# Kernel optimization log

Measured on AMD Instinct MI355X. Metric: run time of the kernel, lower is better.

## Reference

```python
import jax, jax.numpy as jnp
import numpy as np

DIM = 240; NH = 6; HD = 20          # dim, num_heads, head_dim = dim // (2*num_heads)
WS = 16; BWS = 8                    # window size, base window size
R = (WS // BWS) ** 2                # spatial_linear in_features (=4)
LW = WS * WS; LB = BWS * BWS

# static relative-position index for a WSxWS window (same construction as torch buffer)
_coords = np.stack(np.meshgrid(np.arange(WS), np.arange(WS), indexing='ij')).reshape(2, -1)
_rel = (_coords[:, :, None] - _coords[:, None, :]).transpose(1, 2, 0).astype(np.int64)
_rel[..., 0] += WS - 1; _rel[..., 1] += WS - 1; _rel[..., 0] *= 2 * WS - 1
RPI = jnp.asarray(_rel.sum(-1))     # [LW, LW]


def conv2d(x, w, b, pad):
    y = jax.lax.conv_general_dilated(x, w, (1, 1), [(pad, pad), (pad, pad)],
                                     dimension_numbers=('NCHW', 'OIHW', 'NCHW'))
    return y + b[None, :, None, None]


def lrelu(x):
    return jnp.where(x >= 0, x, 0.2 * x)  # LeakyReLU(0.2)


def layer_norm(x, g, b, eps=1e-5):
    m = x.mean(-1, keepdims=True)
    v = jnp.mean((x - m) ** 2, axis=-1, keepdims=True)
    return (x - m) * jax.lax.rsqrt(v + eps) * g + b


def setup_inputs() -> dict:
    key = jax.random.key(0)
    ks = iter(jax.random.split(key, 40))
    rn = lambda shape: jax.random.normal(next(ks), shape, jnp.float32) * 0.02
    B, H, W = 2, 256, 256
    pd = (DIM // 4) // 4  # DynamicPosBias pos_dim = 15
    return {
        'x': jax.random.normal(next(ks), (B, H * W, DIM), jnp.float32),
        # DFE (qv projection)
        'c1_w': rn((DIM // 5, DIM, 1, 1)), 'c1_b': jnp.zeros((DIM // 5,), jnp.float32),
        'c2_w': rn((DIM // 5, DIM // 5, 3, 3)), 'c2_b': jnp.zeros((DIM // 5,), jnp.float32),
        'c3_w': rn((DIM, DIM // 5, 1, 1)), 'c3_b': jnp.zeros((DIM,), jnp.float32),
        'lin_w': rn((DIM, DIM, 1, 1)), 'lin_b': jnp.zeros((DIM,), jnp.float32),
        # spatial linear projection Linear(R, 1)
        'sl_w': rn((1, R)), 'sl_b': jnp.zeros((1,), jnp.float32),
        # DynamicPosBias MLP (residual=False)
        'pp_w': rn((pd, 2)), 'pp_b': jnp.zeros((pd,), jnp.float32),
        'ln1_g': jnp.ones((pd,), jnp.float32), 'ln1_b': jnp.zeros((pd,), jnp.float32),
        'p1_w': rn((pd, pd)), 'p1_b': jnp.zeros((pd,), jnp.float32),
        'ln2_g': jnp.ones((pd,), jnp.float32), 'ln2_b': jnp.zeros((pd,), jnp.float32),
        'p2_w': rn((pd, pd)), 'p2_b': jnp.zeros((pd,), jnp.float32),
        'ln3_g': jnp.ones((pd,), jnp.float32), 'ln3_b': jnp.zeros((pd,), jnp.float32),
        'p3_w': rn((NH, pd)), 'p3_b': jnp.zeros((NH,), jnp.float32),
        # output projection
        'proj_w': rn((DIM, DIM)), 'proj_b': jnp.zeros((DIM,), jnp.float32),
        'H': 256, 'W': 256,
    }


def reference(x, c1_w, c1_b, c2_w, c2_b, c3_w, c3_b, lin_w, lin_b, sl_w, sl_b,
              pp_w, pp_b, ln1_g, ln1_b, p1_w, p1_b, ln2_g, ln2_b, p2_w, p2_b,
              ln3_g, ln3_b, p3_w, p3_b, proj_w, proj_b, H, W):
    B, L, C = x.shape
    # ---- DFE feature projection (conv-gated) ----
    xi = jnp.transpose(x, (0, 2, 1)).reshape(B, C, H, W)
    conv = conv2d(lrelu(conv2d(lrelu(conv2d(xi, c1_w, c1_b, 0)), c2_w, c2_b, 1)), c3_w, c3_b, 0)
    qv = conv * conv2d(xi, lin_w, lin_b, 0)                       # [B,C,H,W]
    qv = jnp.transpose(qv, (0, 2, 3, 1))                          # [B,H,W,C]
    # ---- window partition ----
    nh_w, nw_w = H // WS, W // WS
    qv = qv.reshape(B, nh_w, WS, nw_w, WS, C).transpose(0, 1, 3, 2, 4, 5).reshape(-1, LW, C)
    B_ = qv.shape[0]
    qv = qv.reshape(B_, LW, 2, NH, HD).transpose(2, 0, 3, 1, 4)   # [2,B_,NH,LW,HD]
    q, v = qv[0], qv[1]
    # ---- spatial self-correlation ----
    # spatial linear projection of v: [B_,NH,LW,HD] -> [B_,NH,LB,HD]
    vs = v.reshape(B_, NH, BWS, WS // BWS, BWS, WS // BWS, HD)
    vs = vs.transpose(0, 1, 2, 4, 6, 3, 5).reshape(B_, NH, LB, HD, R)
    vs = jnp.einsum('bnkcr,or->bnkc', vs, sl_w) + sl_b            # Linear(R,1), squeezed
    corr = jnp.einsum('bnlc,bnkc->bnlk', q, vs) / HD              # [B_,NH,LW,LB]
    # dynamic relative position bias (MLP over the mother set of relative coords)
    ph = jnp.arange(1 - WS, WS)
    biases = jnp.stack(jnp.meshgrid(ph, ph, indexing='ij')).reshape(2, -1).T.astype(x.dtype)
    pos = biases @ pp_w.T + pp_b
    pos = jax.nn.relu(layer_norm(pos, ln1_g, ln1_b)) @ p1_w.T + p1_b
    pos = jax.nn.relu(layer_norm(pos, ln2_g, ln2_b)) @ p2_w.T + p2_b
    pos = jax.nn.relu(layer_norm(pos, ln3_g, ln3_b)) @ p3_w.T + p3_b  # [(2*WS-1)^2, NH]
    rpb = jnp.take(pos, RPI.reshape(-1), axis=0).reshape(LW, LW, NH).transpose(2, 0, 1)
    # pool key axis to base-window resolution (consistent with spatial_linear_projection grouping)
    rpb = rpb.reshape(NH, LW, BWS, WS // BWS, BWS, WS // BWS).mean((3, 5)).reshape(NH, LW, LB)
    corr = corr + rpb[None]
    x_s = jnp.einsum('bnlk,bnkc->bnlc', corr, vs)
    x_s = x_s.transpose(0, 2, 1, 3).reshape(B_, LW, NH * HD)      # [B_,LW,C/2]
    # ---- channel self-correlation (single-head over merged channels) ----
    qc = q.transpose(0, 2, 1, 3).reshape(B_, LW, NH * HD)
    vc = v.transpose(0, 2, 1, 3).reshape(B_, LW, NH * HD)
    corr_c = jnp.einsum('blc,bld->bcd', qc, vc) / LW              # [B_,C/2,C/2]
    x_c = jnp.einsum('bcd,bld->blc', corr_c, vc)                  # [B_,LW,C/2]
    # ---- window reverse + spatial-channel fusion ----
    def wrev(t):
        return t.reshape(B, nh_w, nw_w, WS, WS, -1).transpose(0, 1, 3, 2, 4, 5).reshape(B, H, W, -1)
    out = jnp.concatenate([wrev(x_s), wrev(x_c)], axis=-1)        # [B,H,W,C]
    out = out @ proj_w.T + proj_b
    return out.reshape(B, L, C)
```

## Files before the change

kernel.cpp:

```cpp
#include <hip/hip_runtime.h>
#include <math.h>

#define NPIX 131072

typedef __attribute__((ext_vector_type(8))) short bfrag;
typedef __attribute__((ext_vector_type(4))) float facc;
typedef __attribute__((ext_vector_type(4))) unsigned short us4;

__device__ __forceinline__ float lrelu_f(float x) { return x >= 0.f ? x : 0.2f * x; }

__device__ __forceinline__ int pix_of(int w, int l) {
    int b = w >> 8, wi = (w >> 4) & 15, wj = w & 15;
    return ((((b << 4) + wi) * 16 + (l >> 4)) << 8) + (wj << 4) + (l & 15);
}

__device__ __forceinline__ unsigned short bf16rn(float f) {
    unsigned u = __builtin_bit_cast(unsigned, f);
    u += 0x7FFFu + ((u >> 16) & 1u);
    return (unsigned short)(u >> 16);
}
__device__ __forceinline__ float bf16tof(unsigned short h) {
    unsigned u = ((unsigned)h) << 16;
    return __builtin_bit_cast(float, u);
}

__global__ __launch_bounds__(256) void split_x_kernel(const float* __restrict__ x,
                                                      unsigned short* __restrict__ xs2)
{
    int idx = blockIdx.x * 256 + threadIdx.x;
    int row = idx >> 5;
    int k = (idx & 31) * 8;
    float v[8];
    if (k < 240) {
        float4 a = *(const float4*)(x + (size_t)row * 240 + k);
        float4 b = *(const float4*)(x + (size_t)row * 240 + k + 4);
        v[0] = a.x; v[1] = a.y; v[2] = a.z; v[3] = a.w;
        v[4] = b.x; v[5] = b.y; v[6] = b.z; v[7] = b.w;
    } else {
#pragma unroll
        for (int e = 0; e < 8; ++e) v[e] = 0.f;
    }
    bfrag hi, lo;
#pragma unroll
    for (int e = 0; e < 8; ++e) {
        unsigned short h = bf16rn(v[e]);
        hi[e] = (short)h;
        lo[e] = (short)bf16rn(v[e] - bf16tof(h));
    }
    unsigned short* dst = xs2 + (size_t)row * 512 + k;
    *(bfrag*)(dst) = hi;
    *(bfrag*)(dst + 256) = lo;
}

__global__ __launch_bounds__(256) void pack_w_kernel(const float* __restrict__ src,
                                                     int rows, int K,
                                                     unsigned short* __restrict__ dst,
                                                     int total8, int KPAD)
{
    int idx = blockIdx.x * 256 + threadIdx.x;
    if (idx >= total8) return;
    int kper = KPAD >> 3;
    int row = idx / kper;
    int k = (idx - row * kper) * 8;
    float v[8];
#pragma unroll
    for (int e = 0; e < 8; ++e) {
        int kk = k + e;
        v[e] = (row < rows && kk < K) ? src[(size_t)row * K + kk] : 0.f;
    }
    bfrag hi, lo;
#pragma unroll
    for (int e = 0; e < 8; ++e) {
        unsigned short h = bf16rn(v[e]);
        hi[e] = (short)h;
        lo[e] = (short)bf16rn(v[e] - bf16tof(h));
    }
    unsigned short* d = dst + (size_t)row * 2 * KPAD + k;
    *(bfrag*)(d) = hi;
    *(bfrag*)(d + KPAD) = lo;
}

__global__ __launch_bounds__(256) void pack_c2w_kernel(const float* __restrict__ c2_w,
                                                       unsigned short* __restrict__ c2w2)
{
    int idx = blockIdx.x * 256 + threadIdx.x;
    if (idx >= 6912) return;
    int rowid = idx >> 4;
    int c = idx & 15;
    int tap = rowid / 48, n = rowid - tap * 48;
    int ty = tap / 3, tx = tap - ty * 3;
    int lohalf = c >> 3;
    int cbase = (c & 7) * 8;
    bfrag outv;
#pragma unroll
    for (int e = 0; e < 8; ++e) {
        int ci = cbase + e;
        float v = (ci < 48) ? c2_w[(((size_t)n * 48 + ci) * 3 + ty) * 3 + tx] : 0.f;
        unsigned short h = bf16rn(v);
        outv[e] = (short)(lohalf ? bf16rn(v - bf16tof(h)) : h);
    }
    *(bfrag*)(c2w2 + (size_t)rowid * 128 + c * 8) = outv;
}

__device__ __forceinline__ void ln_relu15(const float* h, float* r,
                                          const float* __restrict__ g,
                                          const float* __restrict__ b) {
    float m = 0.f;
#pragma unroll
    for (int f = 0; f < 15; ++f) m += h[f];
    m *= (1.f / 15.f);
    float v = 0.f;
#pragma unroll
    for (int f = 0; f < 15; ++f) { float d = h[f] - m; v += d * d; }
    float rs = rsqrtf(v * (1.f / 15.f) + 1e-5f);
#pragma unroll
    for (int f = 0; f < 15; ++f) {
        float xx = (h[f] - m) * rs * g[f] + b[f];
        r[f] = xx > 0.f ? xx : 0.f;
    }
}

__device__ __forceinline__ void lin15(const float* r, float* h,
                                      const float* __restrict__ w,
                                      const float* __restrict__ b) {
#pragma unroll
    for (int o = 0; o < 15; ++o) {
        float s = b[o];
#pragma unroll
        for (int g = 0; g < 15; ++g) s += r[g] * w[o * 15 + g];
        h[o] = s;
    }
}

__global__ __launch_bounds__(256) void prep_pos_kernel(
    const float* __restrict__ pp_w, const float* __restrict__ pp_b,
    const float* __restrict__ ln1_g, const float* __restrict__ ln1_b,
    const float* __restrict__ p1_w, const float* __restrict__ p1_b,
    const float* __restrict__ ln2_g, const float* __restrict__ ln2_b,
    const float* __restrict__ p2_w, const float* __restrict__ p2_b,
    const float* __restrict__ ln3_g, const float* __restrict__ ln3_b,
    const float* __restrict__ p3_w, const float* __restrict__ p3_b,
    float* __restrict__ pos3)
{
    int tid = threadIdx.x;
    for (int idx = tid; idx < 961; idx += 256) {
        float h[15], r[15];
        float in0 = (float)(idx / 31) - 15.f;
        float in1 = (float)(idx % 31) - 15.f;
#pragma unroll
        for (int f = 0; f < 15; ++f) h[f] = in0 * pp_w[2 * f] + in1 * pp_w[2 * f + 1] + pp_b[f];
        ln_relu15(h, r, ln1_g, ln1_b);
        lin15(r, h, p1_w, p1_b);
        ln_relu15(h, r, ln2_g, ln2_b);
        lin15(r, h, p2_w, p2_b);
        ln_relu15(h, r, ln3_g, ln3_b);
#pragma unroll
        for (int o = 0; o < 6; ++o) {
            float s = p3_b[o];
#pragma unroll
            for (int g = 0; g < 15; ++g) s += r[g] * p3_w[o * 15 + g];
            pos3[idx * 6 + o] = s;
        }
    }
}

__global__ __launch_bounds__(256) void rpb_kernel(const float* __restrict__ pos3,
                                                  float* __restrict__ rpb_t)
{
    int out = blockIdx.x * 256 + threadIdx.x;
    int n = out >> 14;
    int k = (out >> 8) & 63;
    int l = out & 255;
    int a = k >> 3, c = k & 7;
    int i1 = l >> 4, j1 = l & 15;
    float s = 0.f;
#pragma unroll
    for (int bb = 0; bb < 2; ++bb)
#pragma unroll
        for (int d = 0; d < 2; ++d) {
            int i2 = a * 2 + bb, j2 = c * 2 + d;
            int rpi = (i1 - i2 + 15) * 31 + (j1 - j2 + 15);
            s += pos3[rpi * 6 + n];
        }
    rpb_t[out] = s * 0.25f;
}

__device__ __forceinline__ void mfma_kpass3(const unsigned short* __restrict__ A2, int lda2,
                                            const unsigned short* __restrict__ W2, int ldw2,
                                            int ksteps, int mbase, int nbase,
                                            short* lds_a, short* lds_w,
                                            int tid, int wm, int wn,
                                            facc acc[4][4])
{
    int lane = tid & 63;
    int i = lane & 15, g = lane >> 4;
    int kpa = lda2 >> 1, kpw = ldw2 >> 1;
    for (int s = 0; s < ksteps; ++s) {
        int k0 = s * 32;
        {
            int r = tid >> 1, h16 = (tid & 1) * 16;
            const unsigned short* src = A2 + (size_t)(mbase + r) * lda2 + k0 + h16;
            bfrag h0 = *(const bfrag*)(src);
            bfrag h1 = *(const bfrag*)(src + 8);
            bfrag l0 = *(const bfrag*)(src + kpa);
            bfrag l1 = *(const bfrag*)(src + kpa + 8);
            short* dst = lds_a + r * 72 + h16;
            *(bfrag*)(dst)      = h0;  *(bfrag*)(dst + 8)  = h1;
            *(bfrag*)(dst + 32) = l0;  *(bfrag*)(dst + 40) = l1;
        }
        {
            int r = tid >> 1, half = tid & 1;
            const unsigned short* src = W2 + (size_t)(nbase + r) * ldw2 + half * kpw + k0;
            bfrag v0 = *(const bfrag*)(src);
            bfrag v1 = *(const bfrag*)(src + 8);
            bfrag v2 = *(const bfrag*)(src + 16);
            bfrag v3 = *(const bfrag*)(src + 24);
            short* dst = lds_w + r * 72 + half * 32;
            *(bfrag*)(dst)      = v0;  *(bfrag*)(dst + 8)  = v1;
            *(bfrag*)(dst + 16) = v2;  *(bfrag*)(dst + 24) = v3;
        }
        __syncthreads();
        bfrag ah[4], al[4], bh[4], bl[4];
#pragma unroll
        for (int mu = 0; mu < 4; ++mu) {
            const short* p = lds_a + (wm * 64 + mu * 16 + i) * 72 + g * 8;
            ah[mu] = *(const bfrag*)(p);
            al[mu] = *(const bfrag*)(p + 32);
        }
#pragma unroll
        for (int nu = 0; nu < 4; ++nu) {
            const short* p = lds_w + (wn * 64 + nu * 16 + i) * 72 + g * 8;
            bh[nu] = *(const bfrag*)(p);
            bl[nu] = *(const bfrag*)(p + 32);
        }
#pragma unroll
        for (int mu = 0; mu < 4; ++mu)
#pragma unroll
            for (int nu = 0; nu < 4; ++nu) {
                acc[mu][nu] = __builtin_amdgcn_mfma_f32_16x16x32_bf16(ah[mu], bh[nu], acc[mu][nu], 0, 0, 0);
                acc[mu][nu] = __builtin_amdgcn_mfma_f32_16x16x32_bf16(ah[mu], bl[nu], acc[mu][nu], 0, 0, 0);
                acc[mu][nu] = __builtin_amdgcn_mfma_f32_16x16x32_bf16(al[mu], bh[nu], acc[mu][nu], 0, 0, 0);
            }
        __syncthreads();
    }
}

__device__ __forceinline__ void mfma_kpass_n64(const unsigned short* __restrict__ A2, int lda2,
                                               const unsigned short* __restrict__ W2, int ldw2,
                                               int ksteps, int mbase,
                                               short* lds_a, short* lds_w,
                                               int tid, int wm, int wn,
                                               facc acc[4][2])
{
    int lane = tid & 63;
    int i = lane & 15, g = lane >> 4;
    int kpa = lda2 >> 1, kpw = ldw2 >> 1;
    for (int s = 0; s < ksteps; ++s) {
        int k0 = s * 32;
        {
            int r = tid >> 1, h16 = (tid & 1) * 16;
            const unsigned short* src = A2 + (size_t)(mbase + r) * lda2 + k0 + h16;
            bfrag h0 = *(const bfrag*)(src);
            bfrag h1 = *(const bfrag*)(src + 8);
            bfrag l0 = *(const bfrag*)(src + kpa);
            bfrag l1 = *(const bfrag*)(src + kpa + 8);
            short* dst = lds_a + r * 72 + h16;
            *(bfrag*)(dst)      = h0;  *(bfrag*)(dst + 8)  = h1;
            *(bfrag*)(dst + 32) = l0;  *(bfrag*)(dst + 40) = l1;
        }
        if (tid < 128) {
            int r = tid >> 1, half = tid & 1;
            const unsigned short* src = W2 + (size_t)r * ldw2 + half * kpw + k0;
            bfrag v0 = *(const bfrag*)(src);
            bfrag v1 = *(const bfrag*)(src + 8);
            bfrag v2 = *(const bfrag*)(src + 16);
            bfrag v3 = *(const bfrag*)(src + 24);
            short* dst = lds_w + r * 72 + half * 32;
            *(bfrag*)(dst)      = v0;  *(bfrag*)(dst + 8)  = v1;
            *(bfrag*)(dst + 16) = v2;  *(bfrag*)(dst + 24) = v3;
        }
        __syncthreads();
        bfrag ah[4], al[4], bh[2], bl[2];
#pragma unroll
        for (int mu = 0; mu < 4; ++mu) {
            const short* p = lds_a + (wm * 64 + mu * 16 + i) * 72 + g * 8;
            ah[mu] = *(const bfrag*)(p);
            al[mu] = *(const bfrag*)(p + 32);
        }
#pragma unroll
        for (int nu = 0; nu < 2; ++nu) {
            const short* p = lds_w + (wn * 32 + nu * 16 + i) * 72 + g * 8;
            bh[nu] = *(const bfrag*)(p);
            bl[nu] = *(const bfrag*)(p + 32);
        }
#pragma unroll
        for (int mu = 0; mu < 4; ++mu)
#pragma unroll
            for (int nu = 0; nu < 2; ++nu) {
                acc[mu][nu] = __builtin_amdgcn_mfma_f32_16x16x32_bf16(ah[mu], bh[nu], acc[mu][nu], 0, 0, 0);
                acc[mu][nu] = __builtin_amdgcn_mfma_f32_16x16x32_bf16(ah[mu], bl[nu], acc[mu][nu], 0, 0, 0);
                acc[mu][nu] = __builtin_amdgcn_mfma_f32_16x16x32_bf16(al[mu], bh[nu], acc[mu][nu], 0, 0, 0);
            }
        __syncthreads();
    }
}

__global__ __launch_bounds__(256) void conv1_mfma_kernel(const unsigned short* __restrict__ xs2,
    const unsigned short* __restrict__ c1_w2, const float* __restrict__ bias,
    unsigned short* __restrict__ t1s)
{
    __shared__ __align__(16) short lds_a[128 * 72];
    __shared__ __align__(16) short lds_w[64 * 72];
    int tid = threadIdx.x;
    int lane = tid & 63, wid = tid >> 6;
    int wm = wid >> 1, wn = wid & 1;
    int mbase = blockIdx.x * 128;
    facc zero = {0.f, 0.f, 0.f, 0.f};
    facc acc[4][2];
#pragma unroll
    for (int mu = 0; mu < 4; ++mu)
#pragma unroll
        for (int nu = 0; nu < 2; ++nu) acc[mu][nu] = zero;

    mfma_kpass_n64(xs2, 512, c1_w2, 512, 8, mbase, lds_a, lds_w, tid, wm, wn, acc);

    int i = lane & 15, g = lane >> 4;
#pragma unroll
    for (int nu = 0; nu < 2; ++nu) {
        int n = wn * 32 + nu * 16 + i;
        if (n < 48) {
            float bv = bias[n];
#pragma unroll
            for (int mu = 0; mu < 4; ++mu)
#pragma unroll
                for (int rr = 0; rr < 4; ++rr) {
                    size_t m = (size_t)mbase + wm * 64 + mu * 16 + g * 4 + rr;
                    float v = lrelu_f(acc[mu][nu][rr] + bv);
                    unsigned short h = bf16rn(v);
                    t1s[m * 128 + n] = h;
                    t1s[m * 128 + 64 + n] = bf16rn(v - bf16tof(h));
                }
        }
    }
    if (tid < 128) {
        size_t m = (size_t)mbase + tid;
        bfrag z = {0, 0, 0, 0, 0, 0, 0, 0};
        *(bfrag*)(t1s + m * 128 + 48)  = z;
        *(bfrag*)(t1s + m * 128 + 56)  = z;
        *(bfrag*)(t1s + m * 128 + 112) = z;
        *(bfrag*)(t1s + m * 128 + 120) = z;
    }
}

__global__ __launch_bounds__(256) void conv2_mfma_kernel(const unsigned short* __restrict__ t1s,
    const unsigned short* __restrict__ c2w2, const float* __restrict__ bias,
    unsigned short* __restrict__ t2s)
{
    __shared__ __align__(16) short a_s[130 * 128];
    int bid = blockIdx.x;
    int b = bid >> 9;
    int r = (bid >> 1) & 255;
    int half = bid & 1;
    int c0 = half * 128;
    int tid = threadIdx.x;
    int lane = tid & 63, wid = tid >> 6;
    int i = lane & 15, g = lane >> 4;
    facc zero = {0.f, 0.f, 0.f, 0.f};
    facc acc[2][3];
#pragma unroll
    for (int mu = 0; mu < 2; ++mu)
#pragma unroll
        for (int nu = 0; nu < 3; ++nu) acc[mu][nu] = zero;

    for (int dy = 0; dy < 3; ++dy) {
        int grow = r + dy - 1;
        bool rowok = (grow >= 0 && grow < 256);
        for (int idx = tid; idx < 130 * 16; idx += 256) {
            int j = idx >> 4, ch = idx & 15;
            int gc = c0 - 1 + j;
            bfrag v = {0, 0, 0, 0, 0, 0, 0, 0};
            if (rowok && gc >= 0 && gc < 256) {
                size_t gpix = ((size_t)b * 256 + grow) * 256 + gc;
                v = *(const bfrag*)(t1s + gpix * 128 + ch * 8);
            }
            *(bfrag*)&a_s[j * 128 + ((ch ^ (j & 7)) * 8)] = v;
        }
        __syncthreads();
#pragma unroll
        for (int dx = 0; dx < 3; ++dx) {
            const unsigned short* wb = c2w2 + (size_t)(dy * 3 + dx) * 48 * 128;
#pragma unroll
            for (int h = 0; h < 2; ++h) {
                bfrag ah[2], al[2], bh[3], bl[3];
#pragma unroll
                for (int mu = 0; mu < 2; ++mu) {
                    int j = wid * 32 + mu * 16 + i + dx;
                    int chi = (h * 4 + g) ^ (j & 7);
                    int clo = (8 + h * 4 + g) ^ (j & 7);
                    ah[mu] = *(const bfrag*)&a_s[j * 128 + chi * 8];
                    al[mu] = *(const bfrag*)&a_s[j * 128 + clo * 8];
                }
#pragma unroll
                for (int nu = 0; nu < 3; ++nu) {
                    const unsigned short* wp = wb + (size_t)(nu * 16 + i) * 128 + h * 32 + g * 8;
                    bh[nu] = *(const bfrag*)(wp);
                    bl[nu] = *(const bfrag*)(wp + 64);
                }
#pragma unroll
                for (int mu = 0; mu < 2; ++mu)
#pragma unroll
                    for (int nu = 0; nu < 3; ++nu) {
                        acc[mu][nu] = __builtin_amdgcn_mfma_f32_16x16x32_bf16(ah[mu], bh[nu], acc[mu][nu], 0, 0, 0);
                        acc[mu][nu] = __builtin_amdgcn_mfma_f32_16x16x32_bf16(ah[mu], bl[nu], acc[mu][nu], 0, 0, 0);
                        acc[mu][nu] = __builtin_amdgcn_mfma_f32_16x16x32_bf16(al[mu], bh[nu], acc[mu][nu], 0, 0, 0);
                    }
            }
        }
        __syncthreads();
    }
#pragma unroll
    for (int nu = 0; nu < 3; ++nu) {
        int n = nu * 16 + i;
        float bv = bias[n];
#pragma unroll
        for (int mu = 0; mu < 2; ++mu)
#pragma unroll
            for (int rr = 0; rr < 4; ++rr) {
                int lp = wid * 32 + mu * 16 + g * 4 + rr;
                size_t gpix = ((size_t)b * 256 + r) * 256 + (c0 + lp);
                float v = lrelu_f(acc[mu][nu][rr] + bv);
                unsigned short h = bf16rn(v);
                t2s[gpix * 128 + n] = h;
                t2s[gpix * 128 + 64 + n] = bf16rn(v - bf16tof(h));
            }
    }
    if (tid < 128) {
        size_t gpix = ((size_t)b * 256 + r) * 256 + (c0 + tid);
        bfrag z = {0, 0, 0, 0, 0, 0, 0, 0};
        *(bfrag*)(t2s + gpix * 128 + 48)  = z;
        *(bfrag*)(t2s + gpix * 128 + 56)  = z;
        *(bfrag*)(t2s + gpix * 128 + 112) = z;
        *(bfrag*)(t2s + gpix * 128 + 120) = z;
    }
}

__global__ __launch_bounds__(256) void qv_mfma_kernel(const unsigned short* __restrict__ xs2,
    const unsigned short* __restrict__ lin_w2, const float* __restrict__ lin_b,
    const unsigned short* __restrict__ t2s, const unsigned short* __restrict__ c3_w2,
    const float* __restrict__ c3_b, float* __restrict__ qv)
{
    __shared__ __align__(16) short lds_a[128 * 72];
    __shared__ __align__(16) short lds_w[128 * 72];
    int tid = threadIdx.x;
    int lane = tid & 63, wid = tid >> 6;
    int wm = wid >> 1, wn = wid & 1;
    int bid = blockIdx.y * 2 + blockIdx.x;
    int xcd = bid & 7, j = bid >> 3;
    int mbase = (xcd * 128 + (j >> 1)) * 128;
    int nbase = (j & 1) * 128;
    facc zero = {0.f, 0.f, 0.f, 0.f};
    facc acc1[4][4], acc2[4][4];
#pragma unroll
    for (int mu = 0; mu < 4; ++mu)
#pragma unroll
        for (int nu = 0; nu < 4; ++nu) { acc1[mu][nu] = zero; acc2[mu][nu] = zero; }

    mfma_kpass3(xs2, 512, lin_w2, 512, 8, mbase, nbase, lds_a, lds_w, tid, wm, wn, acc1);
    mfma_kpass3(t2s, 128, c3_w2, 128, 2, mbase, nbase, lds_a, lds_w, tid, wm, wn, acc2);

    int i = lane & 15, g = lane >> 4;
#pragma unroll
    for (int nu = 0; nu < 4; ++nu) {
        int n = nbase + wn * 64 + nu * 16 + i;
        if (n < 240) {
            float lb = lin_b[n], cb = c3_b[n];
#pragma unroll
            for (int mu = 0; mu < 4; ++mu)
#pragma unroll
                for (int rr = 0; rr < 4; ++rr) {
                    size_t m = (size_t)mbase + wm * 64 + mu * 16 + g * 4 + rr;
                    qv[m * 240 + n] = (acc2[mu][nu][rr] + cb) * (acc1[mu][nu][rr] + lb);
                }
        }
    }
}

__global__ __launch_bounds__(256) void proj_mfma_kernel(const unsigned short* __restrict__ cat2,
    const unsigned short* __restrict__ proj_w2, const float* __restrict__ bias,
    float* __restrict__ out)
{
    __shared__ __align__(16) short lds_a[128 * 72];
    __shared__ __align__(16) short lds_w[128 * 72];
    int tid = threadIdx.x;
    int lane = tid & 63, wid = tid >> 6;
    int wm = wid >> 1, wn = wid & 1;
    int bid = blockIdx.y * 2 + blockIdx.x;
    int xcd = bid & 7, j = bid >> 3;
    int mbase = (xcd * 128 + (j >> 1)) * 128;
    int nbase = (j & 1) * 128;
    facc zero = {0.f, 0.f, 0.f, 0.f};
    facc acc[4][4];
#pragma unroll
    for (int mu = 0; mu < 4; ++mu)
#pragma unroll
        for (int nu = 0; nu < 4; ++nu) acc[mu][nu] = zero;

    mfma_kpass3(cat2, 512, proj_w2, 512, 8, mbase, nbase, lds_a, lds_w, tid, wm, wn, acc);

    int i = lane & 15, g = lane >> 4;
#pragma unroll
    for (int nu = 0; nu < 4; ++nu) {
        int n = nbase + wn * 64 + nu * 16 + i;
        if (n < 240) {
            float bv = bias[n];
#pragma unroll
            for (int mu = 0; mu < 4; ++mu)
#pragma unroll
                for (int rr = 0; rr < 4; ++rr) {
                    size_t m = (size_t)mbase + wm * 64 + mu * 16 + g * 4 + rr;
                    out[m * 240 + n] = acc[mu][nu][rr] + bv;
                }
        }
    }
}

__global__ __launch_bounds__(256) void xs_kernel(const float* __restrict__ qv,
    const float* __restrict__ rpb_t, const float* __restrict__ sl_w,
    const float* __restrict__ sl_b, unsigned short* __restrict__ cat2)
{
    __shared__ __align__(16) float v_s[256 * 20];
    __shared__ __align__(16) float vs_s[64 * 20];
    int bid = blockIdx.x;
    int xcd = bid & 7;
    int j = bid >> 3;
    int wl = j / 6;
    int n = j - wl * 6;
    int w = xcd * 64 + wl;
    int tid = threadIdx.x;
    int l = tid;
    size_t pix = (size_t)pix_of(w, l);
    const float* qp = qv + pix * 240 + n * 20;
    float qr[20];
#pragma unroll
    for (int h4 = 0; h4 < 5; ++h4) {
        *(float4*)&qr[h4 * 4] = *(const float4*)(qp + h4 * 4);
        *(float4*)&v_s[l * 20 + h4 * 4] = *(const float4*)(qp + 120 + h4 * 4);
    }
    __syncthreads();
    float slw0 = sl_w[0], slw1 = sl_w[1], slw2 = sl_w[2], slw3 = sl_w[3];
    float slb = sl_b[0];
    for (int idx = tid; idx < 1280; idx += 256) {
        int k = idx / 20, hd = idx % 20;
        int a = k >> 3, c = k & 7;
        int l00 = a * 32 + c * 2;
        float vsum = slb
                   + slw0 * v_s[(l00 + 0) * 20 + hd]
                   + slw1 * v_s[(l00 + 1) * 20 + hd]
                   + slw2 * v_s[(l00 + 16) * 20 + hd]
                   + slw3 * v_s[(l00 + 17) * 20 + hd];
        vs_s[idx] = vsum;
    }
    __syncthreads();
    const float* rp = rpb_t + (size_t)n * 16384 + l;
    float acc[20];
#pragma unroll
    for (int hd = 0; hd < 20; ++hd) acc[hd] = 0.f;
#pragma unroll
    for (int k = 0; k < 64; ++k) {
        float vr[20];
#pragma unroll
        for (int h4 = 0; h4 < 5; ++h4)
            *(float4*)&vr[h4 * 4] = *(const float4*)&vs_s[k * 20 + h4 * 4];
        float s0 = 0.f, s1 = 0.f, s2 = 0.f, s3 = 0.f;
#pragma unroll
        for (int hd = 0; hd < 20; hd += 4) {
            s0 += qr[hd + 0] * vr[hd + 0];
            s1 += qr[hd + 1] * vr[hd + 1];
            s2 += qr[hd + 2] * vr[hd + 2];
            s3 += qr[hd + 3] * vr[hd + 3];
        }
        float cc = (s0 + s1 + s2 + s3) * (1.f / 20.f) + rp[(size_t)k * 256];
#pragma unroll
        for (int hd = 0; hd < 20; ++hd) acc[hd] += cc * vr[hd];
    }
    unsigned short* op = cat2 + pix * 512 + n * 20;
#pragma unroll
    for (int h4 = 0; h4 < 5; ++h4) {
        us4 h, lo;
#pragma unroll
        for (int e = 0; e < 4; ++e) {
            float v = acc[h4 * 4 + e];
            unsigned short hh = bf16rn(v);
            h[e] = hh;
            lo[e] = bf16rn(v - bf16tof(hh));
        }
        *(us4*)(op + h4 * 4) = h;
        *(us4*)(op + 256 + h4 * 4) = lo;
    }
    if (n == 0) {
        bfrag z = {0, 0, 0, 0, 0, 0, 0, 0};
        unsigned short* zp = cat2 + pix * 512;
        *(bfrag*)(zp + 240) = z;  *(bfrag*)(zp + 248) = z;
        *(bfrag*)(zp + 496) = z;  *(bfrag*)(zp + 504) = z;
    }
}

__global__ __launch_bounds__(256) void corrc_kernel(const float* __restrict__ qv,
                                                    float* __restrict__ G)
{
    __shared__ __align__(16) float vc_s[16 * 124];
    __shared__ __align__(16) float qc_s[16 * 124];
    int bid = blockIdx.x;
    int w = (bid & 7) * 64 + (bid >> 3);
    int tid = threadIdx.x, ty = tid >> 4, tx = tid & 15;
    float acc[8][8] = {};
    for (int l0 = 0; l0 < 256; l0 += 16) {
        for (int idx = tid; idx < 480; idx += 256) {
            int k = idx / 30, c4 = idx % 30;
            size_t pix = (size_t)pix_of(w, l0 + k);
            const float* qp = qv + pix * 240;
            *(float4*)&qc_s[k * 124 + c4 * 4] = *(const float4*)(qp + c4 * 4);
            *(float4*)&vc_s[k * 124 + c4 * 4] = *(const float4*)(qp + 120 + c4 * 4);
        }
        __syncthreads();
#pragma unroll
        for (int k = 0; k < 16; ++k) {
            float4 a0 = *(const float4*)&vc_s[k * 124 + ty * 8];
            float4 a1 = *(const float4*)&vc_s[k * 124 + ty * 8 + 4];
            float4 b0 = *(const float4*)&qc_s[k * 124 + tx * 8];
            float4 b1 = *(const float4*)&qc_s[k * 124 + tx * 8 + 4];
            float av[8] = {a0.x, a0.y, a0.z, a0.w, a1.x, a1.y, a1.z, a1.w};
            float bv[8] = {b0.x, b0.y, b0.z, b0.w, b1.x, b1.y, b1.z, b1.w};
#pragma unroll
            for (int i = 0; i < 8; ++i)
#pragma unroll
                for (int j = 0; j < 8; ++j) acc[i][j] += av[i] * bv[j];
        }
        __syncthreads();
    }
    float* gp = G + (size_t)w * 14400;
#pragma unroll
    for (int i = 0; i < 8; ++i) {
        int d = ty * 8 + i;
        if (d < 120) {
#pragma unroll
            for (int j4 = 0; j4 < 2; ++j4) {
                int c = tx * 8 + j4 * 4;
                if (c < 120) {
                    float4 o;
                    o.x = acc[i][j4 * 4 + 0]; o.y = acc[i][j4 * 4 + 1];
                    o.z = acc[i][j4 * 4 + 2]; o.w = acc[i][j4 * 4 + 3];
                    *(float4*)(gp + (size_t)d * 120 + c) = o;
                }
            }
        }
    }
}

__global__ __launch_bounds__(256) void xc_kernel(const float* __restrict__ qv,
    const float* __restrict__ G, unsigned short* __restrict__ cat2)
{
    __shared__ __align__(16) float a_s[8 * 132];
    __shared__ __align__(16) float b_s[8 * 124];
    int bid = blockIdx.x;
    int xcd = bid & 7, j = bid >> 3;
    int w = xcd * 64 + (j >> 1);
    int mh = j & 1;
    int tid = threadIdx.x, ty = tid >> 4, tx = tid & 15;
    const float* gp = G + (size_t)w * 14400;
    float acc[8][8] = {};
    for (int k0 = 0; k0 < 120; k0 += 8) {
        {
            int lloc = tid >> 1;
            int kk = (tid & 1) * 4;
            int l = mh * 128 + lloc;
            size_t pix = (size_t)pix_of(w, l);
            float4 v = *(const float4*)(qv + pix * 240 + 120 + k0 + kk);
            a_s[(kk + 0) * 132 + lloc] = v.x;
            a_s[(kk + 1) * 132 + lloc] = v.y;
            a_s[(kk + 2) * 132 + lloc] = v.z;
            a_s[(kk + 3) * 132 + lloc] = v.w;
        }
        if (tid < 240) {
            int k = tid / 30, c4 = tid % 30;
            *(float4*)&b_s[k * 124 + c4 * 4] =
                *(const float4*)(gp + (size_t)(k0 + k) * 120 + c4 * 4);
        }
        __syncthreads();
#pragma unroll
        for (int k = 0; k < 8; ++k) {
            float4 a0 = *(const float4*)&a_s[k * 132 + ty * 8];
            float4 a1 = *(const float4*)&a_s[k * 132 + ty * 8 + 4];
            float4 b0 = *(const float4*)&b_s[k * 124 + tx * 8];
            float4 b1 = *(const float4*)&b_s[k * 124 + tx * 8 + 4];
            float av[8] = {a0.x, a0.y, a0.z, a0.w, a1.x, a1.y, a1.z, a1.w};
            float bv[8] = {b0.x, b0.y, b0.z, b0.w, b1.x, b1.y, b1.z, b1.w};
#pragma unroll
            for (int i = 0; i < 8; ++i)
#pragma unroll
                for (int j2 = 0; j2 < 8; ++j2) acc[i][j2] += av[i] * bv[j2];
        }
        __syncthreads();
    }
#pragma unroll
    for (int i = 0; i < 8; ++i) {
        int l = mh * 128 + ty * 8 + i;
        size_t pix = (size_t)pix_of(w, l);
        unsigned short* op = cat2 + pix * 512;
#pragma unroll
        for (int j4 = 0; j4 < 2; ++j4) {
            int c = tx * 8 + j4 * 4;
            if (c < 120) {
                us4 h, lo;
#pragma unroll
                for (int e = 0; e < 4; ++e) {
                    float v = acc[i][j4 * 4 + e] * (1.f / 256.f);
                    unsigned short hh = bf16rn(v);
                    h[e] = hh;
                    lo[e] = bf16rn(v - bf16tof(hh));
                }
                *(us4*)(op + 120 + c) = h;
                *(us4*)(op + 256 + 120 + c) = lo;
            }
        }
    }
}

extern "C" void kernel_launch(void* const* d_in, const int* in_sizes, int n_in,
                              void* d_out, int out_size, void* d_ws, size_t ws_size,
                              hipStream_t stream)
{
    (void)in_sizes; (void)n_in; (void)out_size;
    const float* x     = (const float*)d_in[0];
    const float* c1_w  = (const float*)d_in[1];
    const float* c1_b  = (const float*)d_in[2];
    const float* c2_w  = (const float*)d_in[3];
    const float* c2_b  = (const float*)d_in[4];
    const float* c3_w  = (const float*)d_in[5];
    const float* c3_b  = (const float*)d_in[6];
    const float* lin_w = (const float*)d_in[7];
    const float* lin_b = (const float*)d_in[8];
    const float* sl_w  = (const float*)d_in[9];
    const float* sl_b  = (const float*)d_in[10];
    const float* pp_w  = (const float*)d_in[11];
    const float* pp_b  = (const float*)d_in[12];
    const float* ln1_g = (const float*)d_in[13];
    const float* ln1_b = (const float*)d_in[14];
    const float* p1_w  = (const float*)d_in[15];
    const float* p1_b  = (const float*)d_in[16];
    const float* ln2_g = (const float*)d_in[17];
    const float* ln2_b = (const float*)d_in[18];
    const float* p2_w  = (const float*)d_in[19];
    const float* p2_b  = (const float*)d_in[20];
    const float* ln3_g = (const float*)d_in[21];
    const float* ln3_b = (const float*)d_in[22];
    const float* p3_w  = (const float*)d_in[23];
    const float* p3_b  = (const float*)d_in[24];
    const float* proj_w = (const float*)d_in[25];
    const float* proj_b = (const float*)d_in[26];

    float* ws = (float*)d_ws;
    float* pos3   = ws;
    float* rpb_t  = ws + 8192;
    unsigned short* lin_w2  = (unsigned short*)(ws + 106496);
    unsigned short* c3_w2   = (unsigned short*)(ws + 172032);
    unsigned short* proj_w2 = (unsigned short*)(ws + 188416);
    unsigned short* c1_w2   = (unsigned short*)(ws + 253952);
    unsigned short* c2w2    = (unsigned short*)(ws + 286720);
    unsigned short* t2s = (unsigned short*)(ws + 314368);
    float* G      = ws + 314368;
    unsigned short* xs2 = (unsigned short*)(ws + 8702976);
    unsigned short* cat2 = xs2;
    float* qvb    = ws + 42257408;
    unsigned short* t1s = (unsigned short*)qvb;
    const size_t required = (size_t)73714688 * 4;
    if (ws_size < required) return;

    pack_w_kernel<<<32, 256, 0, stream>>>(lin_w, 240, 240, lin_w2, 256 * 32, 256);
    pack_w_kernel<<<32, 256, 0, stream>>>(proj_w, 240, 240, proj_w2, 256 * 32, 256);
    pack_w_kernel<<<8, 256, 0, stream>>>(c3_w, 240, 48, c3_w2, 256 * 8, 64);
    pack_w_kernel<<<16, 256, 0, stream>>>(c1_w, 48, 240, c1_w2, 128 * 32, 256);
    pack_c2w_kernel<<<27, 256, 0, stream>>>(c2_w, c2w2);
    split_x_kernel<<<16384, 256, 0, stream>>>(x, xs2);
    prep_pos_kernel<<<1, 256, 0, stream>>>(pp_w, pp_b, ln1_g, ln1_b, p1_w, p1_b,
                                           ln2_g, ln2_b, p2_w, p2_b, ln3_g, ln3_b,
                                           p3_w, p3_b, pos3);
    rpb_kernel<<<384, 256, 0, stream>>>(pos3, rpb_t);
    conv1_mfma_kernel<<<1024, 256, 0, stream>>>(xs2, c1_w2, c1_b, t1s);
    conv2_mfma_kernel<<<1024, 256, 0, stream>>>(t1s, c2w2, c2_b, t2s);
    qv_mfma_kernel<<<dim3(2, 1024), 256, 0, stream>>>(xs2, lin_w2, lin_b, t2s, c3_w2, c3_b, qvb);
    xs_kernel<<<3072, 256, 0, stream>>>(qvb, rpb_t, sl_w, sl_b, cat2);
    corrc_kernel<<<512, 256, 0, stream>>>(qvb, G);
    xc_kernel<<<1024, 256, 0, stream>>>(qvb, G, cat2);
    proj_mfma_kernel<<<dim3(2, 1024), 256, 0, stream>>>(cat2, proj_w2, proj_b, (float*)d_out);
}
```

Measured before the change: 598.5 us.

## Merge weight-pack launches, parallelize pos MLP, remap conv2 blocks per XCD

Five small weight-packing kernels are merged into one launch that dispatches on block index. The positional-bias MLP now spreads its 961 entries across 4 blocks instead of looping inside a single block. The conv2 block index is remapped so each of the 8 XCDs handles a contiguous band of 32 rows, which should improve L2 reuse of the overlapping halo rows. The aim is less launch overhead and better cache locality, while the total work stays the same.

```diff
diff --git a/kernel.cpp b/kernel.cpp
--- a/kernel.cpp
+++ b/kernel.cpp
@@ -52,12 +52,11 @@
     *(bfrag*)(dst + 256) = lo;
 }
 
-__global__ __launch_bounds__(256) void pack_w_kernel(const float* __restrict__ src,
-                                                     int rows, int K,
-                                                     unsigned short* __restrict__ dst,
-                                                     int total8, int KPAD)
-{
-    int idx = blockIdx.x * 256 + threadIdx.x;
+__device__ __forceinline__ void pack_w_body(const float* __restrict__ src,
+                                            int rows, int K,
+                                            unsigned short* __restrict__ dst,
+                                            int total8, int KPAD, int idx)
+{
     if (idx >= total8) return;
     int kper = KPAD >> 3;
     int row = idx / kper;
@@ -80,10 +79,9 @@
     *(bfrag*)(d + KPAD) = lo;
 }
 
-__global__ __launch_bounds__(256) void pack_c2w_kernel(const float* __restrict__ c2_w,
-                                                       unsigned short* __restrict__ c2w2)
-{
-    int idx = blockIdx.x * 256 + threadIdx.x;
+__device__ __forceinline__ void pack_c2w_body(const float* __restrict__ c2_w,
+                                              unsigned short* __restrict__ c2w2, int idx)
+{
     if (idx >= 6912) return;
     int rowid = idx >> 4;
     int c = idx & 15;
@@ -100,6 +98,22 @@
         outv[e] = (short)(lohalf ? bf16rn(v - bf16tof(h)) : h);
     }
     *(bfrag*)(c2w2 + (size_t)rowid * 128 + c * 8) = outv;
+}
+
+__global__ __launch_bounds__(256) void pack_all_kernel(
+    const float* __restrict__ lin_w, const float* __restrict__ proj_w,
+    const float* __restrict__ c3_w, const float* __restrict__ c1_w,
+    const float* __restrict__ c2_w,
+    unsigned short* __restrict__ lin_w2, unsigned short* __restrict__ proj_w2,
+    unsigned short* __restrict__ c3_w2, unsigned short* __restrict__ c1_w2,
+    unsigned short* __restrict__ c2w2)
+{
+    int blk = blockIdx.x, tid = threadIdx.x;
+    if (blk < 32)       pack_w_body(lin_w, 240, 240, lin_w2, 8192, 256, blk * 256 + tid);
+    else if (blk < 64)  pack_w_body(proj_w, 240, 240, proj_w2, 8192, 256, (blk - 32) * 256 + tid);
+    else if (blk < 72)  pack_w_body(c3_w, 240, 48, c3_w2, 2048, 64, (blk - 64) * 256 + tid);
+    else if (blk < 88)  pack_w_body(c1_w, 48, 240, c1_w2, 4096, 256, (blk - 72) * 256 + tid);
+    else                pack_c2w_body(c2_w, c2w2, (blk - 88) * 256 + tid);
 }
 
 __device__ __forceinline__ void ln_relu15(const float* h, float* r,
@@ -142,25 +156,24 @@
     const float* __restrict__ p3_w, const float* __restrict__ p3_b,
     float* __restrict__ pos3)
 {
-    int tid = threadIdx.x;
-    for (int idx = tid; idx < 961; idx += 256) {
-        float h[15], r[15];
-        float in0 = (float)(idx / 31) - 15.f;
-        float in1 = (float)(idx % 31) - 15.f;
-#pragma unroll
-        for (int f = 0; f < 15; ++f) h[f] = in0 * pp_w[2 * f] + in1 * pp_w[2 * f + 1] + pp_b[f];
-        ln_relu15(h, r, ln1_g, ln1_b);
-        lin15(r, h, p1_w, p1_b);
-        ln_relu15(h, r, ln2_g, ln2_b);
-        lin15(r, h, p2_w, p2_b);
-        ln_relu15(h, r, ln3_g, ln3_b);
-#pragma unroll
-        for (int o = 0; o < 6; ++o) {
-            float s = p3_b[o];
-#pragma unroll
-            for (int g = 0; g < 15; ++g) s += r[g] * p3_w[o * 15 + g];
-            pos3[idx * 6 + o] = s;
-        }
+    int idx = blockIdx.x * 256 + threadIdx.x;
+    if (idx >= 961) return;
+    float h[15], r[15];
+    float in0 = (float)(idx / 31) - 15.f;
+    float in1 = (float)(idx % 31) - 15.f;
+#pragma unroll
+    for (int f = 0; f < 15; ++f) h[f] = in0 * pp_w[2 * f] + in1 * pp_w[2 * f + 1] + pp_b[f];
+    ln_relu15(h, r, ln1_g, ln1_b);
+    lin15(r, h, p1_w, p1_b);
+    ln_relu15(h, r, ln2_g, ln2_b);
+    lin15(r, h, p2_w, p2_b);
+    ln_relu15(h, r, ln3_g, ln3_b);
+#pragma unroll
+    for (int o = 0; o < 6; ++o) {
+        float s = p3_b[o];
+#pragma unroll
+        for (int g = 0; g < 15; ++g) s += r[g] * p3_w[o * 15 + g];
+        pos3[idx * 6 + o] = s;
     }
 }
 
@@ -358,9 +371,12 @@
 {
     __shared__ __align__(16) short a_s[130 * 128];
     int bid = blockIdx.x;
-    int b = bid >> 9;
-    int r = (bid >> 1) & 255;
-    int half = bid & 1;
+    int xcd = bid & 7;
+    int j = bid >> 3;
+    int half = j & 1;
+    int rl = (j >> 1) & 31;
+    int b = j >> 6;
+    int r = xcd * 32 + rl;
     int c0 = half * 128;
     int tid = threadIdx.x;
     int lane = tid & 63, wid = tid >> 6;
@@ -376,14 +392,14 @@
         int grow = r + dy - 1;
         bool rowok = (grow >= 0 && grow < 256);
         for (int idx = tid; idx < 130 * 16; idx += 256) {
-            int j = idx >> 4, ch = idx & 15;
-            int gc = c0 - 1 + j;
+            int j2 = idx >> 4, ch = idx & 15;
+            int gc = c0 - 1 + j2;
             bfrag v = {0, 0, 0, 0, 0, 0, 0, 0};
             if (rowok && gc >= 0 && gc < 256) {
                 size_t gpix = ((size_t)b * 256 + grow) * 256 + gc;
                 v = *(const bfrag*)(t1s + gpix * 128 + ch * 8);
             }
-            *(bfrag*)&a_s[j * 128 + ((ch ^ (j & 7)) * 8)] = v;
+            *(bfrag*)&a_s[j2 * 128 + ((ch ^ (j2 & 7)) * 8)] = v;
         }
         __syncthreads();
 #pragma unroll
@@ -394,11 +410,11 @@
                 bfrag ah[2], al[2], bh[3], bl[3];
 #pragma unroll
                 for (int mu = 0; mu < 2; ++mu) {
-                    int j = wid * 32 + mu * 16 + i + dx;
-                    int chi = (h * 4 + g) ^ (j & 7);
-                    int clo = (8 + h * 4 + g) ^ (j & 7);
-                    ah[mu] = *(const bfrag*)&a_s[j * 128 + chi * 8];
-                    al[mu] = *(const bfrag*)&a_s[j * 128 + clo * 8];
+                    int j2 = wid * 32 + mu * 16 + i + dx;
+                    int chi = (h * 4 + g) ^ (j2 & 7);
+                    int clo = (8 + h * 4 + g) ^ (j2 & 7);
+                    ah[mu] = *(const bfrag*)&a_s[j2 * 128 + chi * 8];
+                    al[mu] = *(const bfrag*)&a_s[j2 * 128 + clo * 8];
                 }
 #pragma unroll
                 for (int nu = 0; nu < 3; ++nu) {
@@ -776,13 +792,10 @@
     const size_t required = (size_t)73714688 * 4;
     if (ws_size < required) return;
 
-    pack_w_kernel<<<32, 256, 0, stream>>>(lin_w, 240, 240, lin_w2, 256 * 32, 256);
-    pack_w_kernel<<<32, 256, 0, stream>>>(proj_w, 240, 240, proj_w2, 256 * 32, 256);
-    pack_w_kernel<<<8, 256, 0, stream>>>(c3_w, 240, 48, c3_w2, 256 * 8, 64);
-    pack_w_kernel<<<16, 256, 0, stream>>>(c1_w, 48, 240, c1_w2, 128 * 32, 256);
-    pack_c2w_kernel<<<27, 256, 0, stream>>>(c2_w, c2w2);
+    pack_all_kernel<<<115, 256, 0, stream>>>(lin_w, proj_w, c3_w, c1_w, c2_w,
+                                             lin_w2, proj_w2, c3_w2, c1_w2, c2w2);
     split_x_kernel<<<16384, 256, 0, stream>>>(x, xs2);
-    prep_pos_kernel<<<1, 256, 0, stream>>>(pp_w, pp_b, ln1_g, ln1_b, p1_w, p1_b,
+    prep_pos_kernel<<<4, 256, 0, stream>>>(pp_w, pp_b, ln1_g, ln1_b, p1_w, p1_b,
                                            ln2_g, ln2_b, p2_w, p2_b, ln3_g, ln3_b,
                                            p3_w, p3_b, pos3);
     rpb_kernel<<<384, 256, 0, stream>>>(pos3, rpb_t);
```

Result: faster. 571.4 us (-4.5%).
